# Performance work log

Hardware: AMD Instinct MI355X
Metric: run time of the kernel (lower is better)

The kernel has to match this reference:

```python
import jax, jax.numpy as jnp
import numpy as np

N_HEAD, DK, DV = 16, 64, 64
TEMP = DK ** 0.5
LN_EPS = 1e-5


def setup_inputs() -> dict:
    key = jax.random.key(0)
    ks = jax.random.split(key, 8)
    B, LQ, LK = 8, 1024, 1024
    D1, D2 = 768, 1024
    return {
        'q': jax.random.normal(ks[0], (B, LQ, D1), jnp.float32),
        'k': jax.random.normal(ks[1], (B, LK, D2), jnp.float32),
        'v': jax.random.normal(ks[2], (B, LK, D2), jnp.float32),
        'w_qs': jax.random.normal(ks[3], (D1, N_HEAD * DK), jnp.float32) * 0.02,
        'w_ks': jax.random.normal(ks[4], (D2, N_HEAD * DK), jnp.float32) * 0.02,
        'w_vs': jax.random.normal(ks[5], (D2, N_HEAD * DV), jnp.float32) * 0.02,
        'fc_w': jax.random.normal(ks[6], (N_HEAD * DV, D2), jnp.float32) * 0.02,
        'resid_w': jax.random.normal(ks[7], (D1, N_HEAD * DV), jnp.float32) * 0.02,
        'resid_b': jnp.zeros((N_HEAD * DV,), jnp.float32),
        'ln_gamma': jnp.ones((D2,), jnp.float32),
        'ln_beta': jnp.zeros((D2,), jnp.float32),
    }


def reference(q, k, v, w_qs, w_ks, w_vs, fc_w, resid_w, resid_b, ln_gamma, ln_beta):
    B, LQ, _ = q.shape
    LK = k.shape[1]
    residual = q
    # project and split heads: [B, L, H, d] -> [B, H, L, d]
    Q = (q @ w_qs).reshape(B, LQ, N_HEAD, DK).transpose(0, 2, 1, 3)
    K = (k @ w_ks).reshape(B, LK, N_HEAD, DK).transpose(0, 2, 1, 3)
    V = (v @ w_vs).reshape(B, LK, N_HEAD, DV).transpose(0, 2, 1, 3)
    scores = jnp.einsum('bhqd,bhkd->bhqk', Q / TEMP, K)
    p = jax.nn.softmax(scores, axis=-1)
    # reverse-complement attention (RCA): reverse=True
    p = (1.0 - p) / (LK - 1)
    out = jnp.einsum('bhqk,bhkd->bhqd', p, V)  # dropout is eval-mode identity
    out = out.transpose(0, 2, 1, 3).reshape(B, LQ, N_HEAD * DV)
    out = out @ fc_w
    out = out + (residual @ resid_w + resid_b)
    mean = jnp.mean(out, axis=-1, keepdims=True)
    var = jnp.var(out, axis=-1, keepdims=True)
    out = (out - mean) * jax.lax.rsqrt(var + LN_EPS) * ln_gamma + ln_beta
    return out  # relu=False
```

## Files before the change

### kernel.cpp

```cpp
#include <hip/hip_runtime.h>

typedef __bf16 bf16_t;
typedef __bf16 bf16x8 __attribute__((ext_vector_type(8)));
typedef __bf16 bf16x4 __attribute__((ext_vector_type(4)));
typedef float  f32x4  __attribute__((ext_vector_type(4)));

#if __has_builtin(__builtin_amdgcn_exp2f)
#define EXP2(x) __builtin_amdgcn_exp2f(x)
#else
#define EXP2(x) exp2f(x)
#endif

#define DEVFN __device__ __forceinline__

DEVFN void gl_lds16(void* lds_base, const void* gsrc) {
  __builtin_amdgcn_global_load_lds(
      (const __attribute__((address_space(1))) void*)gsrc,
      (__attribute__((address_space(3))) void*)lds_base, 16, 0, 0);
}

__global__ __launch_bounds__(256) void k_prep(
    const float* __restrict__ q, const float* __restrict__ k, const float* __restrict__ v,
    const float* __restrict__ w_qs, const float* __restrict__ w_ks,
    const float* __restrict__ w_vs, const float* __restrict__ fc_w,
    const float* __restrict__ resid_w,
    bf16_t* __restrict__ qb, bf16_t* __restrict__ kb, bf16_t* __restrict__ vb,
    bf16_t* __restrict__ wqsT, bf16_t* __restrict__ wksT, bf16_t* __restrict__ wvsT,
    bf16_t* __restrict__ fcwT, bf16_t* __restrict__ rswT,
    float* __restrict__ Vs) {
  __shared__ float t[64][65];
  int bid = blockIdx.x;
  if (bid < 1152) {
    const float* w; bf16_t* wt; int K;
    if (bid < 192)      { w = w_qs;    wt = wqsT; K = 768; }
    else if (bid < 448) { w = w_ks;    wt = wksT; K = 1024; bid -= 192; }
    else if (bid < 704) { w = w_vs;    wt = wvsT; K = 1024; bid -= 448; }
    else if (bid < 960) { w = fc_w;    wt = fcwT; K = 1024; bid -= 704; }
    else                { w = resid_w; wt = rswT; K = 768;  bid -= 960; }
    const int bk = (bid >> 4) << 6;
    const int bn = (bid & 15) << 6;
    const int rr = threadIdx.x >> 4;
    const int cc = (threadIdx.x & 15) << 2;
#pragma unroll
    for (int i = 0; i < 4; ++i) {
      int r = i * 16 + rr;
      float4 vv = *reinterpret_cast<const float4*>(&w[(size_t)(bk + r) * 1024 + bn + cc]);
      t[r][cc] = vv.x; t[r][cc + 1] = vv.y; t[r][cc + 2] = vv.z; t[r][cc + 3] = vv.w;
    }
    __syncthreads();
#pragma unroll
    for (int i = 0; i < 4; ++i) {
      int n = i * 16 + rr;
      bf16x4 o;
      o[0] = (bf16_t)t[cc][n];     o[1] = (bf16_t)t[cc + 1][n];
      o[2] = (bf16_t)t[cc + 2][n]; o[3] = (bf16_t)t[cc + 3][n];
      *reinterpret_cast<bf16x4*>(&wt[(size_t)(bn + n) * K + bk + cc]) = o;
    }
    return;
  }
  bid -= 1152;
  if (bid == 0) {
    for (int j = threadIdx.x; j < 8192; j += 256) Vs[j] = 0.f;
  }
  const int NQ = 1572864, NK = 2097152, NT = NQ + 2 * NK;
  int stride = (gridDim.x - 1152) * 256;
  for (int i = bid * 256 + threadIdx.x; i < NT; i += stride) {
    const float* src; bf16_t* dst; int off;
    if (i < NQ)           { src = q; dst = qb; off = i; }
    else if (i < NQ + NK) { src = k; dst = kb; off = i - NQ; }
    else                  { src = v; dst = vb; off = i - NQ - NK; }
    float4 vv = reinterpret_cast<const float4*>(src)[off];
    bf16x4 o;
    o[0] = (bf16_t)vv.x; o[1] = (bf16_t)vv.y; o[2] = (bf16_t)vv.z; o[3] = (bf16_t)vv.w;
    reinterpret_cast<bf16x4*>(dst)[off] = o;
  }
}

DEVFN void gemm_tiles(const bf16_t* __restrict__ A, const bf16_t* __restrict__ Bt,
                      int K, int m0, int n0, bf16_t (*sm)[4096], f32x4 (&acc)[4][4]) {
  const int lane = threadIdx.x & 63;
  const int wv = threadIdx.x >> 6;
  const int wr = (wv >> 1) * 64, wc = (wv & 1) * 64;
  const int lr = lane & 15, lk = lane >> 4;
  const int so0 = wv * 2048 + lane * 16;
  const int so1 = so0 + 1024;
  const int r0 = so0 >> 6, r1 = so1 >> 6;
  const int c0 = ((((so0 >> 4) & 3) ^ (r0 & 3)) << 4);
  const int c1 = ((((so1 >> 4) & 3) ^ (r1 & 3)) << 4);
  const int asw = ((lk ^ (lr & 3)) << 4);
  const char* Apc = (const char*)A;
  const char* Btc = (const char*)Bt;
  f32x4 zro = {0.f, 0.f, 0.f, 0.f};
#pragma unroll
  for (int i = 0; i < 4; ++i)
#pragma unroll
    for (int j = 0; j < 4; ++j) acc[i][j] = zro;

  const int nk = K >> 5;
  auto stage = [&](int buf, int t) {
    gl_lds16((char*)sm[buf] + wv * 2048,        Apc + ((size_t)(m0 + r0) * K + t * 32) * 2 + c0);
    gl_lds16((char*)sm[buf] + wv * 2048 + 1024, Apc + ((size_t)(m0 + r1) * K + t * 32) * 2 + c1);
    gl_lds16((char*)sm[2 + buf] + wv * 2048,        Btc + ((size_t)(n0 + r0) * K + t * 32) * 2 + c0);
    gl_lds16((char*)sm[2 + buf] + wv * 2048 + 1024, Btc + ((size_t)(n0 + r1) * K + t * 32) * 2 + c1);
  };
  stage(0, 0);
  __syncthreads();
  for (int t = 0; t < nk; ++t) {
    const int cur = t & 1;
    if (t + 1 < nk) stage(cur ^ 1, t + 1);
    const char* AsB = (const char*)sm[cur];
    const char* BsB = (const char*)sm[2 + cur];
    bf16x8 af[4], bfr[4];
#pragma unroll
    for (int i = 0; i < 4; ++i)
      af[i] = *(const bf16x8*)(AsB + (wr + i * 16 + lr) * 64 + asw);
#pragma unroll
    for (int j = 0; j < 4; ++j)
      bfr[j] = *(const bf16x8*)(BsB + (wc + j * 16 + lr) * 64 + asw);
#pragma unroll
    for (int i = 0; i < 4; ++i)
#pragma unroll
      for (int j = 0; j < 4; ++j)
        acc[i][j] = __builtin_amdgcn_mfma_f32_16x16x32_bf16(af[i], bfr[j], acc[i][j], 0, 0, 0);
    __syncthreads();
  }
}

__global__ __launch_bounds__(256) void k_gemm_proj(
    const bf16_t* __restrict__ qb, const bf16_t* __restrict__ wqsT, bf16_t* __restrict__ Qp,
    const bf16_t* __restrict__ kb, const bf16_t* __restrict__ wksT, bf16_t* __restrict__ Kp,
    const bf16_t* __restrict__ vb, const bf16_t* __restrict__ wvsT, bf16_t* __restrict__ Vt,
    float* __restrict__ Vsum, float qscale) {
  __shared__ bf16_t sm[4][4096];
  const int bid = blockIdx.x;
  const int route = bid >> 9;
  const int sbid = bid & 511;
  const int wg = (sbid & 7) * 64 + (sbid >> 3);
  const int tn = 8;
  const int m0 = (wg / tn) << 7;
  const int n0 = (wg % tn) << 7;
  const int lane = threadIdx.x & 63;
  const int wv = threadIdx.x >> 6;
  const int wr = (wv >> 1) * 64, wc = (wv & 1) * 64;
  const int lr = lane & 15, lk = lane >> 4;
  f32x4 acc[4][4];

  if (route == 0) {
    gemm_tiles(qb, wqsT, 768, m0, n0, sm, acc);
#pragma unroll
    for (int i = 0; i < 4; ++i)
#pragma unroll
      for (int j = 0; j < 4; ++j)
#pragma unroll
        for (int r = 0; r < 4; ++r)
          Qp[(size_t)(m0 + wr + i * 16 + lk * 4 + r) * 1024 + n0 + wc + j * 16 + lr] =
              (bf16_t)(acc[i][j][r] * qscale);
  } else if (route == 1) {
    gemm_tiles(kb, wksT, 1024, m0, n0, sm, acc);
#pragma unroll
    for (int i = 0; i < 4; ++i)
#pragma unroll
      for (int j = 0; j < 4; ++j)
#pragma unroll
        for (int r = 0; r < 4; ++r)
          Kp[(size_t)(m0 + wr + i * 16 + lk * 4 + r) * 1024 + n0 + wc + j * 16 + lr] =
              (bf16_t)acc[i][j][r];
  } else {
    gemm_tiles(vb, wvsT, 1024, m0, n0, sm, acc);
    const int b = m0 >> 10;
    const int h = (n0 + wc) >> 6;
    const int kt = ((m0 & 1023) + wr) >> 6;
    const size_t tbase = (size_t)(b * 16 + h) * 131072 + (size_t)kt * 8192;
#pragma unroll
    for (int i = 0; i < 4; ++i) {
      const int kvl = i * 16 + lk * 4;
      const int csel = kvl >> 3;
      const int hoff = (kvl & 7) * 2;
#pragma unroll
      for (int j = 0; j < 4; ++j) {
        const int d = j * 16 + lr;
        bf16x4 pw;
#pragma unroll
        for (int r = 0; r < 4; ++r) pw[r] = (bf16_t)acc[i][j][r];
        char* dst = (char*)Vt + tbase + d * 128 + ((csel ^ (d & 7)) << 4) + hoff;
        *reinterpret_cast<bf16x4*>(dst) = pw;
      }
    }
#pragma unroll
    for (int j = 0; j < 4; ++j) {
      float s = 0.f;
#pragma unroll
      for (int i = 0; i < 4; ++i)
#pragma unroll
        for (int r = 0; r < 4; ++r) s += acc[i][j][r];
      s += __shfl_xor(s, 16, 64);
      s += __shfl_xor(s, 32, 64);
      if (lane < 16)
        atomicAdd(&Vsum[(b * 16 + h) * 64 + j * 16 + lane], s);
    }
  }
}

__global__ __launch_bounds__(256) void k_gemm_final(
    const bf16_t* __restrict__ A1, const bf16_t* __restrict__ B1t, int K1,
    const bf16_t* __restrict__ A2, const bf16_t* __restrict__ B2t, int K2,
    const float* __restrict__ bias, bf16_t* __restrict__ Y, int N) {
  __shared__ bf16_t sm[4][4096];
  const int bpx = gridDim.x >> 3;
  const int wg = (blockIdx.x & 7) * bpx + (blockIdx.x >> 3);
  const int tn = N >> 7;
  const int m0 = (wg / tn) << 7;
  const int n0 = (wg % tn) << 7;
  const int lane = threadIdx.x & 63;
  const int wv = threadIdx.x >> 6;
  const int wr = (wv >> 1) * 64, wc = (wv & 1) * 64;
  const int lr = lane & 15, lk = lane >> 4;
  f32x4 acc[4][4];
  f32x4 acc2[4][4];
  gemm_tiles(A1, B1t, K1, m0, n0, sm, acc);
  __syncthreads();
  gemm_tiles(A2, B2t, K2, m0, n0, sm, acc2);
#pragma unroll
  for (int i = 0; i < 4; ++i)
#pragma unroll
    for (int j = 0; j < 4; ++j) {
      float bv = bias[n0 + wc + j * 16 + lr];
#pragma unroll
      for (int r = 0; r < 4; ++r)
        Y[(size_t)(m0 + wr + i * 16 + lk * 4 + r) * N + n0 + wc + j * 16 + lr] =
            (bf16_t)(acc[i][j][r] + acc2[i][j][r] + bv);
    }
}

__global__ __launch_bounds__(512) void k_attn(
    const bf16_t* __restrict__ Qp, const bf16_t* __restrict__ Kp,
    const bf16_t* __restrict__ Vt, const float* __restrict__ Vsum,
    bf16_t* __restrict__ Aout) {
  const int bid = blockIdx.x;
  const int wgid = (bid & 7) * 64 + (bid >> 3);
  const int qg = wgid & 3;
  const int bh = wgid >> 2;
  const int b = bh >> 4, h = bh & 15;
  __shared__ bf16_t Ks[2][4096];
  __shared__ bf16_t Vs[2][4096];
  const int tid = threadIdx.x;
  const int lane = tid & 63;
  const int wv = tid >> 6;
  const int lr = lane & 15, lk = lane >> 4;
  const int stb = (wv >> 2) * 2;
  const int wrow = (wv & 3) * 16;

  const int o = tid * 16;
  const int row = o >> 7;
  const int sc = ((((o >> 4) & 7) ^ (row & 7)) << 4);
  const int srow = (row & 0x23) | ((row & 0x0C) << 1) | ((row & 0x10) >> 2);

  const char* Ksrc  = (const char*)(Kp + ((size_t)(b * 1024 + srow)) * 1024 + h * 64) + sc;
  const char* Vtile = (const char*)Vt + (size_t)bh * 131072 + o;

  gl_lds16((char*)&Ks[0][0] + o, Ksrc);
  gl_lds16((char*)&Vs[0][0] + o, Vtile);

  bf16x8 qa[2][2];
#pragma unroll
  for (int stl = 0; stl < 2; ++stl) {
    const char* qsrc = (const char*)(Qp +
        ((size_t)(b * 1024 + qg * 256 + (stb + stl) * 64 + wrow + lr)) * 1024 + h * 64);
    qa[stl][0] = *(const bf16x8*)(qsrc + lk * 16);
    qa[stl][1] = *(const bf16x8*)(qsrc + 64 + lk * 16);
  }
  __syncthreads();

  const int kb0 = lr * 128 + ((lk ^ (lr & 7)) << 4);
  const int kb1 = lr * 128 + (((4 + lk) ^ (lr & 7)) << 4);
  const int vsw0 = kb0;
  const int vsw1 = kb1;

  f32x4 zro = {0.f, 0.f, 0.f, 0.f};
  f32x4 oacc[2][4];
  f32x4 sum[2];
#pragma unroll
  for (int stl = 0; stl < 2; ++stl) {
    sum[stl] = zro;
#pragma unroll
    for (int g = 0; g < 4; ++g) oacc[stl][g] = zro;
  }
  bf16x8 ones8;
#pragma unroll
  for (int j = 0; j < 8; ++j) ones8[j] = (bf16_t)1.0f;

  for (int kt = 0; kt < 16; ++kt) {
    const int cur = kt & 1;
    const char* KsB = (const char*)&Ks[cur][0];
    const char* VsB = (const char*)&Vs[cur][0];
    if (kt < 15) {
      gl_lds16((char*)&Ks[cur ^ 1][0] + o, Ksrc + (size_t)(kt + 1) * 131072);
      gl_lds16((char*)&Vs[cur ^ 1][0] + o, Vtile + (size_t)(kt + 1) * 8192);
    }

    f32x4 sacc[2][4];
#pragma unroll
    for (int stl = 0; stl < 2; ++stl)
#pragma unroll
      for (int g = 0; g < 4; ++g) sacc[stl][g] = zro;
    {
      bf16x8 kf[4];
#pragma unroll
      for (int g = 0; g < 4; ++g) kf[g] = *(const bf16x8*)(KsB + kb0 + g * 2048);
#pragma unroll
      for (int stl = 0; stl < 2; ++stl)
#pragma unroll
        for (int g = 0; g < 4; ++g)
          sacc[stl][g] = __builtin_amdgcn_mfma_f32_16x16x32_bf16(kf[g], qa[stl][0], sacc[stl][g], 0, 0, 0);
#pragma unroll
      for (int g = 0; g < 4; ++g) kf[g] = *(const bf16x8*)(KsB + kb1 + g * 2048);
#pragma unroll
      for (int stl = 0; stl < 2; ++stl)
#pragma unroll
        for (int g = 0; g < 4; ++g)
          sacc[stl][g] = __builtin_amdgcn_mfma_f32_16x16x32_bf16(kf[g], qa[stl][1], sacc[stl][g], 0, 0, 0);
    }

    bf16x8 pa[2][2];
#pragma unroll
    for (int stl = 0; stl < 2; ++stl)
#pragma unroll
      for (int c = 0; c < 2; ++c) {
        bf16x8 pw;
#pragma unroll
        for (int r = 0; r < 4; ++r) {
          pw[r]     = (bf16_t)EXP2(sacc[stl][2 * c][r]);
          pw[4 + r] = (bf16_t)EXP2(sacc[stl][2 * c + 1][r]);
        }
        pa[stl][c] = pw;
      }

#pragma unroll
    for (int c = 0; c < 2; ++c) {
      const int vb = (c == 0) ? vsw0 : vsw1;
      bf16x8 vf[4];
#pragma unroll
      for (int gd = 0; gd < 4; ++gd)
        vf[gd] = *(const bf16x8*)(VsB + vb + gd * 2048);
#pragma unroll
      for (int stl = 0; stl < 2; ++stl) {
        sum[stl] = __builtin_amdgcn_mfma_f32_16x16x32_bf16(pa[stl][c], ones8, sum[stl], 0, 0, 0);
#pragma unroll
        for (int gd = 0; gd < 4; ++gd)
          oacc[stl][gd] = __builtin_amdgcn_mfma_f32_16x16x32_bf16(pa[stl][c], vf[gd], oacc[stl][gd], 0, 0, 0);
      }
    }
    __syncthreads();
  }

  float vs_d[4];
#pragma unroll
  for (int gd = 0; gd < 4; ++gd) vs_d[gd] = Vsum[bh * 64 + gd * 16 + lr];
#pragma unroll
  for (int stl = 0; stl < 2; ++stl) {
    float inv[4];
#pragma unroll
    for (int r = 0; r < 4; ++r) inv[r] = 1.0f / sum[stl][r];
#pragma unroll
    for (int gd = 0; gd < 4; ++gd)
#pragma unroll
      for (int r = 0; r < 4; ++r) {
        int d = gd * 16 + lr;
        int qrow = qg * 256 + (stb + stl) * 64 + wrow + lk * 4 + r;
        float attnv = oacc[stl][gd][r] * inv[r];
        float val = (vs_d[gd] - attnv) * (1.0f / 1023.0f);
        Aout[((size_t)(b * 1024 + qrow)) * 1024 + h * 64 + d] = (bf16_t)val;
      }
  }
}

__global__ __launch_bounds__(256) void k_ln(
    const bf16_t* __restrict__ Y, const float* __restrict__ gamma,
    const float* __restrict__ beta, float* __restrict__ out) {
  const int row = blockIdx.x, tid = threadIdx.x;
  bf16x4 xv = reinterpret_cast<const bf16x4*>(Y + (size_t)row * 1024)[tid];
  float x0 = (float)xv[0], x1 = (float)xv[1], x2 = (float)xv[2], x3 = (float)xv[3];
  float s = x0 + x1 + x2 + x3;
  float q = x0 * x0 + x1 * x1 + x2 * x2 + x3 * x3;
#pragma unroll
  for (int off = 32; off > 0; off >>= 1) {
    s += __shfl_xor(s, off, 64);
    q += __shfl_xor(q, off, 64);
  }
  __shared__ float ss[4], qs[4];
  if ((tid & 63) == 0) { ss[tid >> 6] = s; qs[tid >> 6] = q; }
  __syncthreads();
  s = ss[0] + ss[1] + ss[2] + ss[3];
  q = qs[0] + qs[1] + qs[2] + qs[3];
  float mean = s * (1.f / 1024.f);
  float var = q * (1.f / 1024.f) - mean * mean;
  float rstd = rsqrtf(var + 1e-5f);
  float4 g = reinterpret_cast<const float4*>(gamma)[tid];
  float4 bt = reinterpret_cast<const float4*>(beta)[tid];
  float4 o;
  o.x = (x0 - mean) * rstd * g.x + bt.x;
  o.y = (x1 - mean) * rstd * g.y + bt.y;
  o.z = (x2 - mean) * rstd * g.z + bt.z;
  o.w = (x3 - mean) * rstd * g.w + bt.w;
  reinterpret_cast<float4*>(out + (size_t)row * 1024)[tid] = o;
}

extern "C" void kernel_launch(void* const* d_in, const int* in_sizes, int n_in,
                              void* d_out, int out_size, void* d_ws, size_t ws_size,
                              hipStream_t stream) {
  (void)in_sizes; (void)n_in; (void)out_size;
  const float* q       = (const float*)d_in[0];
  const float* k       = (const float*)d_in[1];
  const float* v       = (const float*)d_in[2];
  const float* w_qs    = (const float*)d_in[3];
  const float* w_ks    = (const float*)d_in[4];
  const float* w_vs    = (const float*)d_in[5];
  const float* fc_w    = (const float*)d_in[6];
  const float* resid_w = (const float*)d_in[7];
  const float* resid_b = (const float*)d_in[8];
  const float* ln_g    = (const float*)d_in[9];
  const float* ln_b    = (const float*)d_in[10];
  float* out = (float*)d_out;
  char* ws = (char*)d_ws;

  if (ws_size < (size_t)122716160) return;

  bf16_t* qb   = (bf16_t*)(ws + 0);
  bf16_t* kb   = (bf16_t*)(ws + 12582912);
  bf16_t* vb   = (bf16_t*)(ws + 29360128);
  bf16_t* Y    = (bf16_t*)(ws + 12582912);
  bf16_t* wqsT = (bf16_t*)(ws + 46137344);
  bf16_t* wksT = (bf16_t*)(ws + 47710208);
  bf16_t* wvsT = (bf16_t*)(ws + 49807360);
  bf16_t* fcwT = (bf16_t*)(ws + 51904512);
  bf16_t* rswT = (bf16_t*)(ws + 54001664);
  bf16_t* Qp   = (bf16_t*)(ws + 55574528);
  bf16_t* Kp   = (bf16_t*)(ws + 72351744);
  bf16_t* Aout = (bf16_t*)(ws + 89128960);
  bf16_t* VtT  = (bf16_t*)(ws + 105906176);
  float*  Vsm  = (float*)(ws + 122683392);

  k_prep<<<3200, 256, 0, stream>>>(q, k, v, w_qs, w_ks, w_vs, fc_w, resid_w,
                                   qb, kb, vb, wqsT, wksT, wvsT, fcwT, rswT, Vsm);
  k_gemm_proj<<<1536, 256, 0, stream>>>(qb, wqsT, Qp, kb, wksT, Kp, vb, wvsT, VtT,
                                        Vsm, 0.18033688011f);
  k_attn<<<512, 512, 0, stream>>>(Qp, Kp, VtT, Vsm, Aout);
  k_gemm_final<<<512, 256, 0, stream>>>(Aout, fcwT, 1024, qb, rswT, 768, resid_b, Y, 1024);
  k_ln<<<8192, 256, 0, stream>>>(Y, ln_g, ln_b, out);
}
```

Measured before the change: 178.8 us.

## Stage V tiles through LDS, reorder projection routes, single-accumulator final GEMM

Result: no change. 177.2 us (-0.9%).

```diff
diff --git a/kernel.cpp b/kernel.cpp
--- a/kernel.cpp
+++ b/kernel.cpp
@@ -146,31 +146,12 @@
   f32x4 acc[4][4];
 
   if (route == 0) {
-    gemm_tiles(qb, wqsT, 768, m0, n0, sm, acc);
-#pragma unroll
-    for (int i = 0; i < 4; ++i)
-#pragma unroll
-      for (int j = 0; j < 4; ++j)
-#pragma unroll
-        for (int r = 0; r < 4; ++r)
-          Qp[(size_t)(m0 + wr + i * 16 + lk * 4 + r) * 1024 + n0 + wc + j * 16 + lr] =
-              (bf16_t)(acc[i][j][r] * qscale);
-  } else if (route == 1) {
-    gemm_tiles(kb, wksT, 1024, m0, n0, sm, acc);
-#pragma unroll
-    for (int i = 0; i < 4; ++i)
-#pragma unroll
-      for (int j = 0; j < 4; ++j)
-#pragma unroll
-        for (int r = 0; r < 4; ++r)
-          Kp[(size_t)(m0 + wr + i * 16 + lk * 4 + r) * 1024 + n0 + wc + j * 16 + lr] =
-              (bf16_t)acc[i][j][r];
-  } else {
     gemm_tiles(vb, wvsT, 1024, m0, n0, sm, acc);
     const int b = m0 >> 10;
-    const int h = (n0 + wc) >> 6;
-    const int kt = ((m0 & 1023) + wr) >> 6;
-    const size_t tbase = (size_t)(b * 16 + h) * 131072 + (size_t)kt * 8192;
+    const int h0 = n0 >> 6;
+    const int kt0 = (m0 & 1023) >> 6;
+    const int h_local = wc >> 6, kt_local = wr >> 6;
+    char* tl = (char*)sm + (h_local * 2 + kt_local) * 8192;
 #pragma unroll
     for (int i = 0; i < 4; ++i) {
       const int kvl = i * 16 + lk * 4;
@@ -182,10 +163,18 @@
         bf16x4 pw;
 #pragma unroll
         for (int r = 0; r < 4; ++r) pw[r] = (bf16_t)acc[i][j][r];
-        char* dst = (char*)Vt + tbase + d * 128 + ((csel ^ (d & 7)) << 4) + hoff;
-        *reinterpret_cast<bf16x4*>(dst) = pw;
+        *reinterpret_cast<bf16x4*>(tl + d * 128 + ((csel ^ (d & 7)) << 4) + hoff) = pw;
       }
     }
+    {
+      const size_t gbase = (size_t)(b * 16 + h0 + h_local) * 131072 +
+                           (size_t)(kt0 + kt_local) * 8192;
+#pragma unroll
+      for (int it = 0; it < 8; ++it)
+        *reinterpret_cast<uint4*>((char*)Vt + gbase + it * 1024 + lane * 16) =
+            *reinterpret_cast<const uint4*>(tl + it * 1024 + lane * 16);
+    }
+    const int h = h0 + h_local;
 #pragma unroll
     for (int j = 0; j < 4; ++j) {
       float s = 0.f;
@@ -198,6 +187,26 @@
       if (lane < 16)
         atomicAdd(&Vsum[(b * 16 + h) * 64 + j * 16 + lane], s);
     }
+  } else if (route == 1) {
+    gemm_tiles(kb, wksT, 1024, m0, n0, sm, acc);
+#pragma unroll
+    for (int i = 0; i < 4; ++i)
+#pragma unroll
+      for (int j = 0; j < 4; ++j)
+#pragma unroll
+        for (int r = 0; r < 4; ++r)
+          Kp[(size_t)(m0 + wr + i * 16 + lk * 4 + r) * 1024 + n0 + wc + j * 16 + lr] =
+              (bf16_t)acc[i][j][r];
+  } else {
+    gemm_tiles(qb, wqsT, 768, m0, n0, sm, acc);
+#pragma unroll
+    for (int i = 0; i < 4; ++i)
+#pragma unroll
+      for (int j = 0; j < 4; ++j)
+#pragma unroll
+        for (int r = 0; r < 4; ++r)
+          Qp[(size_t)(m0 + wr + i * 16 + lk * 4 + r) * 1024 + n0 + wc + j * 16 + lr] =
+              (bf16_t)(acc[i][j][r] * qscale);
   }
 }
 
@@ -215,11 +224,51 @@
   const int wv = threadIdx.x >> 6;
   const int wr = (wv >> 1) * 64, wc = (wv & 1) * 64;
   const int lr = lane & 15, lk = lane >> 4;
+  const int so0 = wv * 2048 + lane * 16;
+  const int so1 = so0 + 1024;
+  const int r0 = so0 >> 6, r1 = so1 >> 6;
+  const int c0 = ((((so0 >> 4) & 3) ^ (r0 & 3)) << 4);
+  const int c1 = ((((so1 >> 4) & 3) ^ (r1 & 3)) << 4);
+  const int asw = ((lk ^ (lr & 3)) << 4);
+  f32x4 zro = {0.f, 0.f, 0.f, 0.f};
   f32x4 acc[4][4];
-  f32x4 acc2[4][4];
-  gemm_tiles(A1, B1t, K1, m0, n0, sm, acc);
+#pragma unroll
+  for (int i = 0; i < 4; ++i)
+#pragma unroll
+    for (int j = 0; j < 4; ++j) acc[i][j] = zro;
+
+  const int nk1 = K1 >> 5;
+  const int nkt = (K1 + K2) >> 5;
+  auto stage = [&](int buf, int t) {
+    const char* Apc; const char* Btc; int K, tt;
+    if (t < nk1) { Apc = (const char*)A1; Btc = (const char*)B1t; K = K1; tt = t; }
+    else         { Apc = (const char*)A2; Btc = (const char*)B2t; K = K2; tt = t - nk1; }
+    gl_lds16((char*)sm[buf] + wv * 2048,        Apc + ((size_t)(m0 + r0) * K + tt * 32) * 2 + c0);
+    gl_lds16((char*)sm[buf] + wv * 2048 + 1024, Apc + ((size_t)(m0 + r1) * K + tt * 32) * 2 + c1);
+    gl_lds16((char*)sm[2 + buf] + wv * 2048,        Btc + ((size_t)(n0 + r0) * K + tt * 32) * 2 + c0);
+    gl_lds16((char*)sm[2 + buf] + wv * 2048 + 1024, Btc + ((size_t)(n0 + r1) * K + tt * 32) * 2 + c1);
+  };
+  stage(0, 0);
   __syncthreads();
-  gemm_tiles(A2, B2t, K2, m0, n0, sm, acc2);
+  for (int t = 0; t < nkt; ++t) {
+    const int cur = t & 1;
+    if (t + 1 < nkt) stage(cur ^ 1, t + 1);
+    const char* AsB = (const char*)sm[cur];
+    const char* BsB = (const char*)sm[2 + cur];
+    bf16x8 af[4], bfr[4];
+#pragma unroll
+    for (int i = 0; i < 4; ++i)
+      af[i] = *(const bf16x8*)(AsB + (wr + i * 16 + lr) * 64 + asw);
+#pragma unroll
+    for (int j = 0; j < 4; ++j)
+      bfr[j] = *(const bf16x8*)(BsB + (wc + j * 16 + lr) * 64 + asw);
+#pragma unroll
+    for (int i = 0; i < 4; ++i)
+#pragma unroll
+      for (int j = 0; j < 4; ++j)
+        acc[i][j] = __builtin_amdgcn_mfma_f32_16x16x32_bf16(af[i], bfr[j], acc[i][j], 0, 0, 0);
+    __syncthreads();
+  }
 #pragma unroll
   for (int i = 0; i < 4; ++i)
 #pragma unroll
@@ -228,7 +277,7 @@
 #pragma unroll
       for (int r = 0; r < 4; ++r)
         Y[(size_t)(m0 + wr + i * 16 + lk * 4 + r) * N + n0 + wc + j * 16 + lr] =
-            (bf16_t)(acc[i][j][r] + acc2[i][j][r] + bv);
+            (bf16_t)(acc[i][j][r] + bv);
     }
 }
 
@@ -273,8 +322,6 @@
 
   const int kb0 = lr * 128 + ((lk ^ (lr & 7)) << 4);
   const int kb1 = lr * 128 + (((4 + lk) ^ (lr & 7)) << 4);
-  const int vsw0 = kb0;
-  const int vsw1 = kb1;
 
   f32x4 zro = {0.f, 0.f, 0.f, 0.f};
   f32x4 oacc[2][4];
@@ -337,7 +384,7 @@
 
 #pragma unroll
     for (int c = 0; c < 2; ++c) {
-      const int vb = (c == 0) ? vsw0 : vsw1;
+      const int vb = (c == 0) ? kb0 : kb1;
       bf16x8 vf[4];
 #pragma unroll
       for (int gd = 0; gd < 4; ++gd)
```
